# Kernel optimization log

Measured on AMD Instinct MI355X. Metric: run time of the kernel, lower is better.

The kernel has to match this reference:

```python
import jax, jax.numpy as jnp
import numpy as np

D_MODEL = 1024
STATE = 16
EXPAND = 2
D_INNER = D_MODEL * EXPAND
KCONV = 4


def setup_inputs() -> dict:
    key = jax.random.key(0)
    ks = jax.random.split(key, 8)
    s = 0.02  # small init scale for stability
    return {
        "x": jax.random.normal(ks[0], (2, 2048, D_MODEL), jnp.float32),
        "W_in": jax.random.normal(ks[1], (2 * D_INNER, D_MODEL), jnp.float32) * s,
        "conv_w": jax.random.normal(ks[2], (D_INNER, 1, KCONV), jnp.float32) * s,
        "conv_b": jnp.zeros((D_INNER,), jnp.float32),
        # A negative so exp(delta*A) <= 1 (stable recurrence, as in real Mamba init)
        "A": -jnp.abs(jax.random.normal(ks[3], (D_INNER, STATE), jnp.float32)),
        "W_x": jax.random.normal(ks[4], (2 * STATE + 1, D_INNER), jnp.float32) * s,
        "W_dt": jax.random.normal(ks[5], (D_INNER, 1), jnp.float32) * s,
        "b_dt": jnp.zeros((D_INNER,), jnp.float32),
        "W_out": jax.random.normal(ks[6], (D_MODEL, D_INNER), jnp.float32) * s,
    }


def reference(x, W_in, conv_w, conv_b, A, W_x, W_dt, b_dt, W_out):
    B, L, _ = x.shape
    N = A.shape[1]

    # in_proj, split into x-branch and gate z
    xz = jnp.einsum('bld,ed->ble', x, W_in)            # (B,L,2*d_inner)
    xi, z = jnp.split(xz, 2, axis=-1)

    # causal depthwise conv1d (torch: pad=3, kernel=4, truncate to L == left-pad 3, valid)
    xc = jnp.transpose(xi, (0, 2, 1))                  # (B,d_inner,L)
    xc = jnp.pad(xc, ((0, 0), (0, 0), (KCONV - 1, 0)))
    xc = jax.lax.conv_general_dilated(
        xc, conv_w, window_strides=(1,), padding='VALID',
        dimension_numbers=('NCH', 'OIH', 'NCH'),
        feature_group_count=conv_w.shape[0])
    xc = xc + conv_b[None, :, None]
    u = jax.nn.silu(jnp.transpose(xc, (0, 2, 1)))      # (B,L,d_inner)

    # input-dependent delta, B, C
    x_dbl = jnp.einsum('bld,ed->ble', u, W_x)          # (B,L,2N+1)
    dlt, Bm, Cm = jnp.split(x_dbl, [1, 1 + N], axis=-1)
    delta = jax.nn.softplus(dlt @ W_dt.T + b_dt)       # (B,L,d_inner)

    # selective scan over time
    def step(h, inp):
        u_t, d_t, B_t, C_t = inp                       # (B,d),(B,d),(B,N),(B,N)
        A_bar = jnp.exp(d_t[..., None] * A)            # (B,d,N)
        h = A_bar * h + (d_t * u_t)[..., None] * B_t[:, None, :]
        y = jnp.einsum('bdn,bn->bd', h, C_t)
        return h, y

    h0 = jnp.zeros((B, A.shape[0], N), u.dtype)
    xs = (jnp.swapaxes(u, 0, 1), jnp.swapaxes(delta, 0, 1),
          jnp.swapaxes(Bm, 0, 1), jnp.swapaxes(Cm, 0, 1))
    _, ys = jax.lax.scan(step, h0, xs)                 # ys: (L,B,d_inner)
    y = jnp.swapaxes(ys, 0, 1)

    y = y * jax.nn.silu(z)
    return jnp.einsum('bld,md->blm', y, W_out)
```

## Files before the change

kernel.cpp:

```cpp
#include <hip/hip_runtime.h>
#include <hip/hip_bf16.h>

#define BATCH   2
#define LSEQ    2048
#define DMODEL  1024
#define DINNER  2048
#define NST     16

#define LC      32
#define NCHUNK  (LSEQ / LC)

#define LOG2E   1.4426950408889634f
#define RLOG2E  0.6931471805599453f

typedef __bf16 bf16x8 __attribute__((ext_vector_type(8)));
typedef float  f32x4  __attribute__((ext_vector_type(4)));

__device__ __forceinline__ unsigned short f2bf(float f) {
  unsigned int u = __float_as_uint(f);
  return (unsigned short)((u + 0x7FFFu + ((u >> 16) & 1u)) >> 16);
}

__device__ __forceinline__ float fast_exp2(float x) {
#if __has_builtin(__builtin_amdgcn_exp2f)
  return __builtin_amdgcn_exp2f(x);
#else
  float r; asm("v_exp_f32 %0, %1\ns_nop 0" : "=v"(r) : "v"(x)); return r;
#endif
}
__device__ __forceinline__ float fast_log2(float x) {
#if __has_builtin(__builtin_amdgcn_logf)
  return __builtin_amdgcn_logf(x);
#else
  float r; asm("v_log_f32 %0, %1\ns_nop 0" : "=v"(r) : "v"(x)); return r;
#endif
}
__device__ __forceinline__ float fast_softplus(float x) {
  float ex = fast_exp2(x * LOG2E);
  return fast_log2(1.0f + ex) * RLOG2E;
}

__device__ __forceinline__ void async_copy16(const void* g, void* l) {
  __builtin_amdgcn_global_load_lds((__attribute__((address_space(1))) void*)g,
                                   (__attribute__((address_space(3))) void*)l,
                                   16, 0, 0);
}

__global__ __launch_bounds__(256) void cvt_tri(const float4* __restrict__ a,
                                               ushort4* __restrict__ oa, int na4,
                                               const float4* __restrict__ b,
                                               ushort4* __restrict__ ob, int nb4,
                                               const float4* __restrict__ c,
                                               ushort4* __restrict__ oc, int nc4) {
  int i = blockIdx.x * 256 + threadIdx.x;
  if (i < na4) {
    float4 v = a[i];
    ushort4 r; r.x = f2bf(v.x); r.y = f2bf(v.y); r.z = f2bf(v.z); r.w = f2bf(v.w);
    oa[i] = r;
  } else if (i - na4 < nb4) {
    int j = i - na4;
    float4 v = b[j];
    ushort4 r; r.x = f2bf(v.x); r.y = f2bf(v.y); r.z = f2bf(v.z); r.w = f2bf(v.w);
    ob[j] = r;
  } else if (i - na4 - nb4 < nc4) {
    int j = i - na4 - nb4;
    float4 v = c[j];
    ushort4 r; r.x = f2bf(v.x); r.y = f2bf(v.y); r.z = f2bf(v.z); r.w = f2bf(v.w);
    oc[j] = r;
  }
}

template<int N, int BN, int K, int NSPLIT>
__global__ __launch_bounds__(256, 2) void gemm_bf16(const unsigned short* __restrict__ A,
                                                    const unsigned short* __restrict__ B,
                                                    float* __restrict__ C0,
                                                    float* __restrict__ C1) {
  constexpr int NB = BN / 32;
  __shared__ unsigned short As[128][64];
  __shared__ unsigned short Bs[BN][64];
  const int tid  = threadIdx.x;
  const int wave = tid >> 6;
  const int lane = tid & 63;
  const int row0 = blockIdx.y * 128;
  const int col0 = blockIdx.x * BN;
  const int wr   = (wave >> 1) * 64;
  const int wc   = (wave & 1)  * (BN / 2);
  const int fr   = lane & 15;
  const int fq   = lane >> 4;

  f32x4 acc[4][NB] = {};

  const int sr  = wave * 8 + (lane >> 3);
  const int gp  = lane & 7;
  const int sgl = gp ^ (sr & 7);
  const unsigned short* gA = A + (size_t)(row0 + sr) * K + sgl * 8;
  const unsigned short* gB = B + (size_t)(col0 + sr) * K + sgl * 8;
  char* lA = (char*)As + wave * 1024;
  char* lB = (char*)Bs + wave * 1024;

  const int rsw = (fr & 7);

  for (int k0 = 0; k0 < K; k0 += 64) {
    #pragma unroll
    for (int c = 0; c < 4; ++c)
      async_copy16(gA + (size_t)c * 32 * K + k0, lA + c * 4096);
    #pragma unroll
    for (int c = 0; c < NB; ++c)
      async_copy16(gB + (size_t)c * 32 * K + k0, lB + c * 4096);
    __syncthreads();

    #pragma unroll
    for (int kk = 0; kk < 2; ++kk) {
      bf16x8 af[4], bfr[NB];
      #pragma unroll
      for (int i = 0; i < 4; ++i)
        af[i] = *(const bf16x8*)((const char*)As + (wr + i * 16 + fr) * 128 +
                                 (((kk << 2) | fq) ^ rsw) * 16);
      #pragma unroll
      for (int j = 0; j < NB; ++j)
        bfr[j] = *(const bf16x8*)((const char*)Bs + (wc + j * 16 + fr) * 128 +
                                  (((kk << 2) | fq) ^ rsw) * 16);
      #pragma unroll
      for (int i = 0; i < 4; ++i)
        #pragma unroll
        for (int j = 0; j < NB; ++j)
          acc[i][j] = __builtin_amdgcn_mfma_f32_16x16x32_bf16(af[i], bfr[j], acc[i][j], 0, 0, 0);
    }
    __syncthreads();
  }

  float* Cb;
  int cb, cstride;
  if (col0 < NSPLIT) { Cb = C0; cb = col0;          cstride = NSPLIT; }
  else               { Cb = C1; cb = col0 - NSPLIT; cstride = N - NSPLIT; }

  #pragma unroll
  for (int i = 0; i < 4; ++i)
    #pragma unroll
    for (int j = 0; j < NB; ++j) {
      int row = row0 + wr + i * 16 + fq * 4;
      int col = cb + wc + j * 16 + fr;
      #pragma unroll
      for (int r = 0; r < 4; ++r)
        Cb[(size_t)(row + r) * cstride + col] = acc[i][j][r];
    }
}

__global__ __launch_bounds__(256) void conv_kernel(const float* __restrict__ xi,
                                                   const float* __restrict__ cw,
                                                   const float* __restrict__ cb,
                                                   float* __restrict__ u) {
  size_t i = (size_t)blockIdx.x * 256 + threadIdx.x;
  int d4 = (int)(i & (DINNER / 4 - 1));
  int t2 = (int)((i >> 9) & (LSEQ / 2 - 1));
  int b  = (int)(i >> 19);
  int d  = d4 * 4;
  int t0 = t2 * 2;

  float4 w0 = *(const float4*)(cw + (d + 0) * 4);
  float4 w1 = *(const float4*)(cw + (d + 1) * 4);
  float4 w2 = *(const float4*)(cw + (d + 2) * 4);
  float4 w3 = *(const float4*)(cw + (d + 3) * 4);
  float4 bias = *(const float4*)(cb + d);

  size_t base = ((size_t)b * LSEQ + t0) * DINNER + d;
  const float4 zero = make_float4(0.f, 0.f, 0.f, 0.f);
  float4 xm3 = (t0 >= 3) ? *(const float4*)(xi + base - 3 * DINNER) : zero;
  float4 xm2 = (t0 >= 2) ? *(const float4*)(xi + base - 2 * DINNER) : zero;
  float4 xm1 = (t0 >= 1) ? *(const float4*)(xi + base - 1 * DINNER) : zero;
  float4 x00 = *(const float4*)(xi + base);
  float4 xp1 = *(const float4*)(xi + base + DINNER);

  float4 s0, s1;
  s0.x = bias.x + w0.x * xm3.x + w0.y * xm2.x + w0.z * xm1.x + w0.w * x00.x;
  s0.y = bias.y + w1.x * xm3.y + w1.y * xm2.y + w1.z * xm1.y + w1.w * x00.y;
  s0.z = bias.z + w2.x * xm3.z + w2.y * xm2.z + w2.z * xm1.z + w2.w * x00.z;
  s0.w = bias.w + w3.x * xm3.w + w3.y * xm2.w + w3.z * xm1.w + w3.w * x00.w;
  s1.x = bias.x + w0.x * xm2.x + w0.y * xm1.x + w0.z * x00.x + w0.w * xp1.x;
  s1.y = bias.y + w1.x * xm2.y + w1.y * xm1.y + w1.z * x00.y + w1.w * xp1.y;
  s1.z = bias.z + w2.x * xm2.z + w2.y * xm1.z + w2.z * x00.z + w2.w * xp1.z;
  s1.w = bias.w + w3.x * xm2.w + w3.y * xm1.w + w3.z * x00.w + w3.w * xp1.w;

  float4 r0, r1;
  r0.x = s0.x / (1.0f + __expf(-s0.x));
  r0.y = s0.y / (1.0f + __expf(-s0.y));
  r0.z = s0.z / (1.0f + __expf(-s0.z));
  r0.w = s0.w / (1.0f + __expf(-s0.w));
  r1.x = s1.x / (1.0f + __expf(-s1.x));
  r1.y = s1.y / (1.0f + __expf(-s1.y));
  r1.z = s1.z / (1.0f + __expf(-s1.z));
  r1.w = s1.w / (1.0f + __expf(-s1.w));

  *(float4*)(u + base)          = r0;
  *(float4*)(u + base + DINNER) = r1;
}

__global__ __launch_bounds__(256, 2) void xdbl_kernel(const float* __restrict__ u,
                                                      const float* __restrict__ Wx,
                                                      float* __restrict__ dltbuf,
                                                      float* __restrict__ bc) {
  const int tid  = threadIdx.x;
  const int wave = tid >> 6;
  const int lane = tid & 63;
  const int row0 = blockIdx.x * 4;

  float acc[9][4];
  #pragma unroll
  for (int i = 0; i < 9; ++i)
    #pragma unroll
    for (int r = 0; r < 4; ++r) acc[i][r] = 0.0f;

  const float* up    = u  + (size_t)row0 * DINNER + lane * 4;
  const float* wbase = Wx + (size_t)wave * 8 * DINNER + lane * 4;
  const float* w32   = Wx + (size_t)32 * DINNER + lane * 4;

  for (int kt = 0; kt < 8; ++kt) {
    const int ko = kt * 256;
    float4 uv0 = *(const float4*)(up + 0 * DINNER + ko);
    float4 uv1 = *(const float4*)(up + 1 * DINNER + ko);
    float4 uv2 = *(const float4*)(up + 2 * DINNER + ko);
    float4 uv3 = *(const float4*)(up + 3 * DINNER + ko);
    #pragma unroll
    for (int i = 0; i < 9; ++i) {
      float4 w = (i < 8) ? *(const float4*)(wbase + (size_t)i * DINNER + ko)
                         : *(const float4*)(w32 + ko);
      acc[i][0] = fmaf(uv0.x, w.x, fmaf(uv0.y, w.y, fmaf(uv0.z, w.z, fmaf(uv0.w, w.w, acc[i][0]))));
      acc[i][1] = fmaf(uv1.x, w.x, fmaf(uv1.y, w.y, fmaf(uv1.z, w.z, fmaf(uv1.w, w.w, acc[i][1]))));
      acc[i][2] = fmaf(uv2.x, w.x, fmaf(uv2.y, w.y, fmaf(uv2.z, w.z, fmaf(uv2.w, w.w, acc[i][2]))));
      acc[i][3] = fmaf(uv3.x, w.x, fmaf(uv3.y, w.y, fmaf(uv3.z, w.z, fmaf(uv3.w, w.w, acc[i][3]))));
    }
  }

  #pragma unroll
  for (int i = 0; i < 9; ++i)
    #pragma unroll
    for (int r = 0; r < 4; ++r)
      #pragma unroll
      for (int m = 1; m < 64; m <<= 1)
        acc[i][r] += __shfl_xor(acc[i][r], m);

  #pragma unroll
  for (int r = 0; r < 4; ++r) {
    if (lane == r) {
      const size_t row = row0 + r;
      #pragma unroll
      for (int i = 0; i < 8; ++i) {
        const int e = wave * 8 + i;
        if (e == 0) dltbuf[row] = acc[i][r];
        else        bc[row * 32 + (e - 1)] = acc[i][r];
      }
      if (wave == 0) bc[row * 32 + 31] = acc[8][r];
    }
  }
}

__global__ __launch_bounds__(256) void scanA(const float* __restrict__ u,
                                             const float* __restrict__ dltbuf,
                                             const float* __restrict__ bc,
                                             const float* __restrict__ Amat,
                                             const float* __restrict__ Wdt,
                                             const float* __restrict__ bdt,
                                             float* __restrict__ Sbuf,
                                             float* __restrict__ Wbuf) {
  __shared__ float sB[LC][16];
  __shared__ float sdlt[LC];
  const int tid  = threadIdx.x;
  const int dblk = blockIdx.x & 7;
  const int c    = (blockIdx.x >> 3) & (NCHUNK - 1);
  const int b    = blockIdx.x >> 9;
  const int d    = dblk * 256 + tid;
  const int t0   = c * LC;

  if (tid < LC * 4) {
    int r = tid >> 2, cp = (tid & 3) * 4;
    *(float4*)&sB[r][cp] = *(const float4*)(bc + ((size_t)(b * LSEQ + t0) + r) * 32 + cp);
  }
  if (tid < LC) sdlt[tid] = dltbuf[(size_t)b * LSEQ + t0 + tid];

  const float wd = Wdt[d];
  const float bd = bdt[d];
  float A2[16];
  #pragma unroll
  for (int i = 0; i < 4; ++i) {
    float4 v = *(const float4*)(Amat + (size_t)d * 16 + i * 4);
    A2[i*4+0] = v.x * LOG2E; A2[i*4+1] = v.y * LOG2E;
    A2[i*4+2] = v.z * LOG2E; A2[i*4+3] = v.w * LOG2E;
  }
  float h[16];
  #pragma unroll
  for (int n = 0; n < 16; ++n) h[n] = 0.0f;
  float S = 0.0f;

  size_t gu = ((size_t)b * LSEQ + t0) * DINNER + d;
  float u0 = u[gu], u1 = u[gu + DINNER];
  __syncthreads();

  auto body = [&](float uc, int ttl) {
    float dl = fast_softplus(fmaf(sdlt[ttl], wd, bd));
    float Bv[16];
    *(float4*)&Bv[0]  = *(const float4*)&sB[ttl][0];
    *(float4*)&Bv[4]  = *(const float4*)&sB[ttl][4];
    *(float4*)&Bv[8]  = *(const float4*)&sB[ttl][8];
    *(float4*)&Bv[12] = *(const float4*)&sB[ttl][12];
    S += dl;
    float dlu = dl * uc;
    #pragma unroll
    for (int n = 0; n < 16; ++n) {
      float ab = fast_exp2(dl * A2[n]);
      h[n] = fmaf(ab, h[n], dlu * Bv[n]);
    }
  };

  for (int tt = 0; tt < LC; tt += 2) {
    float u2 = u[gu + 2 * DINNER], u3 = u[gu + 3 * DINNER];
    body(u0, tt);
    body(u1, tt + 1);
    u0 = u2; u1 = u3;
    gu += 2 * DINNER;
  }

  const size_t gc = (size_t)(b * DINNER + d);
  Sbuf[gc * NCHUNK + c] = S;
  size_t o = (gc * NCHUNK + c) * 16;
  #pragma unroll
  for (int i = 0; i < 4; ++i)
    *(float4*)(Wbuf + o + i * 4) = make_float4(h[i*4], h[i*4+1], h[i*4+2], h[i*4+3]);
}

__global__ __launch_bounds__(256) void scanB(const float* __restrict__ Sbuf,
                                             float* __restrict__ Wbuf,
                                             const float* __restrict__ Amat) {
  const int lane_id = blockIdx.x * 256 + threadIdx.x;
  const int gc = lane_id >> 4;
  const int n  = lane_id & 15;
  const int d  = gc & (DINNER - 1);
  const float A2 = Amat[(size_t)d * 16 + n] * LOG2E;
  const float* sp = Sbuf + (size_t)gc * NCHUNK;
  const size_t wbase = (size_t)gc * NCHUNK * 16 + n;
  float h = 0.0f;
  #pragma unroll 8
  for (int c = 0; c < NCHUNK; ++c) {
    float P = fast_exp2(A2 * sp[c]);
    float hin = h;
    h = fmaf(P, h, Wbuf[wbase + (size_t)c * 16]);
    Wbuf[wbase + (size_t)c * 16] = hin;
  }
}

__global__ __launch_bounds__(256) void scanC(const float* __restrict__ u,
                                             const float* __restrict__ zz,
                                             const float* __restrict__ dltbuf,
                                             const float* __restrict__ bc,
                                             const float* __restrict__ Amat,
                                             const float* __restrict__ Wdt,
                                             const float* __restrict__ bdt,
                                             const float* __restrict__ Hin,
                                             unsigned short* __restrict__ ybf) {
  __shared__ float sbc[LC][32];
  __shared__ float sdlt[LC];
  const int tid  = threadIdx.x;
  const int dblk = blockIdx.x & 7;
  const int c    = (blockIdx.x >> 3) & (NCHUNK - 1);
  const int b    = blockIdx.x >> 9;
  const int d    = dblk * 256 + tid;
  const int t0   = c * LC;

  ((float4*)sbc)[tid] = ((const float4*)(bc + ((size_t)b * LSEQ + t0) * 32))[tid];
  if (tid < LC) sdlt[tid] = dltbuf[(size_t)b * LSEQ + t0 + tid];

  const float wd = Wdt[d];
  const float bd = bdt[d];
  float A2[16];
  #pragma unroll
  for (int i = 0; i < 4; ++i) {
    float4 v = *(const float4*)(Amat + (size_t)d * 16 + i * 4);
    A2[i*4+0] = v.x * LOG2E; A2[i*4+1] = v.y * LOG2E;
    A2[i*4+2] = v.z * LOG2E; A2[i*4+3] = v.w * LOG2E;
  }
  const size_t o = ((size_t)(b * DINNER + d) * NCHUNK + c) * 16;
  float h[16];
  #pragma unroll
  for (int i = 0; i < 4; ++i) {
    float4 v = *(const float4*)(Hin + o + i * 4);
    h[i*4+0] = v.x; h[i*4+1] = v.y; h[i*4+2] = v.z; h[i*4+3] = v.w;
  }

  size_t gu = ((size_t)b * LSEQ + t0) * DINNER + d;

  float u0 = u[gu],  u1 = u[gu + DINNER];
  float z0 = zz[gu], z1 = zz[gu + DINNER];
  __syncthreads();

  auto body = [&](float uc, float zc, int ttl, size_t cu) {
    float dl = fast_softplus(fmaf(sdlt[ttl], wd, bd));
    float Bv[16], Cv[16];
    *(float4*)&Bv[0]  = *(const float4*)&sbc[ttl][0];
    *(float4*)&Bv[4]  = *(const float4*)&sbc[ttl][4];
    *(float4*)&Bv[8]  = *(const float4*)&sbc[ttl][8];
    *(float4*)&Bv[12] = *(const float4*)&sbc[ttl][12];
    *(float4*)&Cv[0]  = *(const float4*)&sbc[ttl][16];
    *(float4*)&Cv[4]  = *(const float4*)&sbc[ttl][20];
    *(float4*)&Cv[8]  = *(const float4*)&sbc[ttl][24];
    *(float4*)&Cv[12] = *(const float4*)&sbc[ttl][28];
    float dlu = dl * uc;
    float y = 0.0f;
    #pragma unroll
    for (int n = 0; n < 16; ++n) {
      float ab = fast_exp2(dl * A2[n]);
      h[n] = fmaf(ab, h[n], dlu * Bv[n]);
      y = fmaf(h[n], Cv[n], y);
    }
    float sig = 1.0f / (1.0f + __expf(-zc));
    ybf[cu] = f2bf(y * zc * sig);
  };

  for (int tt = 0; tt < LC; tt += 2) {
    float u2 = u[gu + 2 * DINNER],  u3 = u[gu + 3 * DINNER];
    float z2 = zz[gu + 2 * DINNER], z3 = zz[gu + 3 * DINNER];
    body(u0, z0, tt,     gu);
    body(u1, z1, tt + 1, gu + DINNER);
    u0 = u2; u1 = u3; z0 = z2; z1 = z3;
    gu += 2 * DINNER;
  }
}

extern "C" void kernel_launch(void* const* d_in, const int* in_sizes, int n_in,
                              void* d_out, int out_size, void* d_ws, size_t ws_size,
                              hipStream_t stream) {
  const float* x      = (const float*)d_in[0];
  const float* W_in   = (const float*)d_in[1];
  const float* conv_w = (const float*)d_in[2];
  const float* conv_b = (const float*)d_in[3];
  const float* A      = (const float*)d_in[4];
  const float* W_x    = (const float*)d_in[5];
  const float* W_dt   = (const float*)d_in[6];
  const float* b_dt   = (const float*)d_in[7];
  const float* W_out  = (const float*)d_in[8];
  float* out = (float*)d_out;

  float* ws  = (float*)d_ws;
  float* xi  = ws;
  float* zz  = xi  + (size_t)BATCH * LSEQ * DINNER;
  float* u   = zz  + (size_t)BATCH * LSEQ * DINNER;
  float* bc  = u   + (size_t)BATCH * LSEQ * DINNER;
  float* Sb  = bc  + (size_t)BATCH * LSEQ * 32;
  float* dlt = Sb  + (size_t)BATCH * DINNER * NCHUNK;
  float* Wb  = dlt + (size_t)BATCH * LSEQ;

  const int ML = BATCH * LSEQ;

  unsigned short* x_bf    = (unsigned short*)Wb;
  unsigned short* win_bf  = (unsigned short*)Wb + (size_t)ML * DMODEL;
  unsigned short* ybf     = (unsigned short*)xi;
  unsigned short* wout_bf = (unsigned short*)(Wb + (size_t)BATCH * DINNER * NCHUNK * 16);

  const int na4 = ML * DMODEL / 4, nb4 = 2 * DINNER * DMODEL / 4, nc4 = DMODEL * DINNER / 4;
  cvt_tri<<<(na4 + nb4 + nc4 + 255) / 256, 256, 0, stream>>>(
      (const float4*)x, (ushort4*)x_bf, na4,
      (const float4*)W_in, (ushort4*)win_bf, nb4,
      (const float4*)W_out, (ushort4*)wout_bf, nc4);
  gemm_bf16<2 * DINNER, 128, DMODEL, DINNER><<<dim3((2 * DINNER) / 128, ML / 128), 256, 0, stream>>>(
      x_bf, win_bf, xi, zz);
  conv_kernel<<<(ML * DINNER / 8) / 256, 256, 0, stream>>>(xi, conv_w, conv_b, u);
  xdbl_kernel<<<ML / 4, 256, 0, stream>>>(u, W_x, dlt, bc);
  scanA<<<BATCH * NCHUNK * 8, 256, 0, stream>>>(u, dlt, bc, A, W_dt, b_dt, Sb, Wb);
  scanB<<<(BATCH * DINNER * NST) / 256, 256, 0, stream>>>(Sb, Wb, A);
  scanC<<<BATCH * NCHUNK * 8, 256, 0, stream>>>(u, zz, dlt, bc, A, W_dt, b_dt, Wb, ybf);
  gemm_bf16<DMODEL, 32, DINNER, DMODEL><<<dim3(DMODEL / 32, ML / 128), 256, 0, stream>>>(
      ybf, wout_bf, out, out);
}
```

Baseline: 198.1 us.

## Replace in_proj GEMM with 256x256-tile 8-wave double-buffered async-LDS kernel

Adds a new bf16 MFMA GEMM for the input projection. It uses 512 threads, 256x256 output tiles, an XOR-swizzled LDS layout, and two 32-deep K stages filled by global_load_lds async copies, with explicit waitcnt, barriers and setprio around the MFMA bursts. The larger tile raises data reuse per LDS load and the double buffering overlaps global loads with compute, cutting memory traffic and stalls in the largest GEMM. In exchange the grid shrinks to 256 blocks at one block per CU, and the 64KB LDS plus 128 accumulator registers per thread limit occupancy.

```diff
diff --git a/kernel.cpp b/kernel.cpp
--- a/kernel.cpp
+++ b/kernel.cpp
@@ -45,6 +45,8 @@
                                    (__attribute__((address_space(3))) void*)l,
                                    16, 0, 0);
 }
+
+#define SCHED0 __builtin_amdgcn_sched_barrier(0)
 
 __global__ __launch_bounds__(256) void cvt_tri(const float4* __restrict__ a,
                                                ushort4* __restrict__ oa, int na4,
@@ -70,6 +72,115 @@
   }
 }
 
+__global__ __launch_bounds__(512, 1) void gemm8p(const unsigned short* __restrict__ A,
+                                                 const unsigned short* __restrict__ B,
+                                                 float* __restrict__ C0,
+                                                 float* __restrict__ C1) {
+  constexpr int K = 1024;
+  __shared__ char lds[65536];
+  const int tid  = threadIdx.x;
+  const int lane = tid & 63;
+  const int wave = tid >> 6;
+  const int fr   = lane & 15;
+  const int fq   = lane >> 4;
+  const int wr   = (wave >> 2) * 128;
+  const int wc   = (wave & 3) * 64;
+  const int row0 = blockIdx.y * 256;
+  const int col0 = blockIdx.x * 256;
+
+  f32x4 acc[8][4] = {};
+
+  const int i0 = tid, i1 = tid + 512;
+  const int r0 = i0 >> 2, g0 = i0 & 3;
+  const int r1 = i1 >> 2, g1 = i1 & 3;
+  const unsigned short* gA0 = A + (size_t)(row0 + r0) * K + (g0 ^ (r0 & 3)) * 8;
+  const unsigned short* gA1 = A + (size_t)(row0 + r1) * K + (g1 ^ (r1 & 3)) * 8;
+  const unsigned short* gB0 = B + (size_t)(col0 + r0) * K + (g0 ^ (r0 & 3)) * 8;
+  const unsigned short* gB1 = B + (size_t)(col0 + r1) * K + (g1 ^ (r1 & 3)) * 8;
+  char* const dA0 = lds + (i0 - lane) * 16;
+  char* const dA1 = lds + (i1 - lane) * 16;
+  char* const dB0 = lds + 16384 + (i0 - lane) * 16;
+  char* const dB1 = lds + 16384 + (i1 - lane) * 16;
+
+  auto STAGE = [&](int kt, int sb) {
+    const int k0 = kt * 32;
+    async_copy16(gA0 + k0, dA0 + sb);
+    async_copy16(gA1 + k0, dA1 + sb);
+    async_copy16(gB0 + k0, dB0 + sb);
+    async_copy16(gB1 + k0, dB1 + sb);
+  };
+
+  const int swz = (fq ^ (fr & 3)) * 16;
+  auto COMPUTE = [&](int sb) {
+    const char* LA = lds + sb;
+    const char* LB = lds + sb + 16384;
+    bf16x8 bfrg[4], afrg[4];
+    #pragma unroll
+    for (int j = 0; j < 4; ++j)
+      bfrg[j] = *(const bf16x8*)(LB + (wc + j * 16 + fr) * 64 + swz);
+    #pragma unroll
+    for (int i = 0; i < 4; ++i)
+      afrg[i] = *(const bf16x8*)(LA + (wr + i * 16 + fr) * 64 + swz);
+    __builtin_amdgcn_s_setprio(1);
+    #pragma unroll
+    for (int i = 0; i < 4; ++i)
+      #pragma unroll
+      for (int j = 0; j < 4; ++j)
+        acc[i][j] = __builtin_amdgcn_mfma_f32_16x16x32_bf16(afrg[i], bfrg[j], acc[i][j], 0, 0, 0);
+    __builtin_amdgcn_s_setprio(0);
+    #pragma unroll
+    for (int i = 0; i < 4; ++i)
+      afrg[i] = *(const bf16x8*)(LA + (wr + (i + 4) * 16 + fr) * 64 + swz);
+    __builtin_amdgcn_s_setprio(1);
+    #pragma unroll
+    for (int i = 0; i < 4; ++i)
+      #pragma unroll
+      for (int j = 0; j < 4; ++j)
+        acc[i + 4][j] = __builtin_amdgcn_mfma_f32_16x16x32_bf16(afrg[i], bfrg[j], acc[i + 4][j], 0, 0, 0);
+    __builtin_amdgcn_s_setprio(0);
+  };
+
+  STAGE(0, 0);
+  STAGE(1, 32768);
+  asm volatile("s_waitcnt vmcnt(4)" ::: "memory"); SCHED0;
+  __builtin_amdgcn_s_barrier(); SCHED0;
+
+  for (int tp = 0; tp < 16; ++tp) {
+    COMPUTE(0);
+    __builtin_amdgcn_s_barrier(); SCHED0;
+    if (tp < 15) {
+      STAGE(2 * tp + 2, 0);
+      asm volatile("s_waitcnt vmcnt(4)" ::: "memory");
+    } else {
+      asm volatile("s_waitcnt vmcnt(0)" ::: "memory");
+    }
+    SCHED0;
+    __builtin_amdgcn_s_barrier(); SCHED0;
+
+    COMPUTE(32768);
+    if (tp == 15) break;
+    __builtin_amdgcn_s_barrier(); SCHED0;
+    STAGE(2 * tp + 3, 32768);
+    asm volatile("s_waitcnt vmcnt(4)" ::: "memory");
+    SCHED0;
+    __builtin_amdgcn_s_barrier(); SCHED0;
+  }
+
+  float* Cb; int cb;
+  if (col0 < DINNER) { Cb = C0; cb = col0; }
+  else               { Cb = C1; cb = col0 - DINNER; }
+  #pragma unroll
+  for (int i = 0; i < 8; ++i)
+    #pragma unroll
+    for (int j = 0; j < 4; ++j) {
+      int row = row0 + wr + i * 16 + fq * 4;
+      int col = cb + wc + j * 16 + fr;
+      #pragma unroll
+      for (int r = 0; r < 4; ++r)
+        Cb[(size_t)(row + r) * DINNER + col] = acc[i][j][r];
+    }
+}
+
 template<int N, int BN, int K, int NSPLIT>
 __global__ __launch_bounds__(256, 2) void gemm_bf16(const unsigned short* __restrict__ A,
                                                     const unsigned short* __restrict__ B,
@@ -459,8 +570,7 @@
       (const float4*)x, (ushort4*)x_bf, na4,
       (const float4*)W_in, (ushort4*)win_bf, nb4,
       (const float4*)W_out, (ushort4*)wout_bf, nc4);
-  gemm_bf16<2 * DINNER, 128, DMODEL, DINNER><<<dim3((2 * DINNER) / 128, ML / 128), 256, 0, stream>>>(
-      x_bf, win_bf, xi, zz);
+  gemm8p<<<dim3(16, 16), 512, 0, stream>>>(x_bf, win_bf, xi, zz);
   conv_kernel<<<(ML * DINNER / 8) / 256, 256, 0, stream>>>(xi, conv_w, conv_b, u);
   xdbl_kernel<<<ML / 4, 256, 0, stream>>>(u, W_x, dlt, bc);
   scanA<<<BATCH * NCHUNK * 8, 256, 0, stream>>>(u, dlt, bc, A, W_dt, b_dt, Sb, Wb);
```

After: 202.4 us. 2.2% more time.

## Fuse causal depthwise conv and SiLU into in_proj GEMM epilogue

Applied to the files above, without the earlier changes.

The in_proj GEMM epilogue now applies the causal depthwise conv and SiLU directly on the accumulator tile, using lane shuffles to fetch the three previous timesteps within each 64-row tile. Only the boundary rows at tile edges are stored raw, and a small conv_fix kernel recomputes the first three rows of each 64-row tile. This removes the full fp32 xi write and reread plus the separate conv pass. In exchange the epilogue does more ALU work and makes scattered partial stores, and correctness depends on the cross-wave boundary bookkeeping.

```diff
diff --git a/kernel.cpp b/kernel.cpp
--- a/kernel.cpp
+++ b/kernel.cpp
@@ -38,6 +38,10 @@
 __device__ __forceinline__ float fast_softplus(float x) {
   float ex = fast_exp2(x * LOG2E);
   return fast_log2(1.0f + ex) * RLOG2E;
+}
+
+__device__ __forceinline__ float silu(float x) {
+  return x / (1.0f + __expf(-x));
 }
 
 __device__ __forceinline__ void async_copy16(const void* g, void* l) {
@@ -70,11 +74,14 @@
   }
 }
 
-template<int N, int BN, int K, int NSPLIT>
+template<int N, int BN, int K, int NSPLIT, bool FUSE>
 __global__ __launch_bounds__(256, 2) void gemm_bf16(const unsigned short* __restrict__ A,
                                                     const unsigned short* __restrict__ B,
                                                     float* __restrict__ C0,
-                                                    float* __restrict__ C1) {
+                                                    float* __restrict__ C1,
+                                                    const float* __restrict__ cw,
+                                                    const float* __restrict__ cbs,
+                                                    float* __restrict__ xiraw) {
   constexpr int NB = BN / 32;
   __shared__ unsigned short As[128][64];
   __shared__ unsigned short Bs[BN][64];
@@ -129,70 +136,99 @@
     __syncthreads();
   }
 
-  float* Cb;
-  int cb, cstride;
-  if (col0 < NSPLIT) { Cb = C0; cb = col0;          cstride = NSPLIT; }
-  else               { Cb = C1; cb = col0 - NSPLIT; cstride = N - NSPLIT; }
-
-  #pragma unroll
-  for (int i = 0; i < 4; ++i)
+  if (FUSE && col0 < NSPLIT) {
+    const int src = (lane + 48) & 63;
     #pragma unroll
     for (int j = 0; j < NB; ++j) {
-      int row = row0 + wr + i * 16 + fq * 4;
-      int col = cb + wc + j * 16 + fr;
-      #pragma unroll
-      for (int r = 0; r < 4; ++r)
-        Cb[(size_t)(row + r) * cstride + col] = acc[i][j][r];
+      const int d = col0 + wc + j * 16 + fr;
+      const float4 w = *(const float4*)(cw + d * 4);
+      const float cb0 = cbs[d];
+      float pr1 = 0.f, pr2 = 0.f, pr3 = 0.f;
+      #pragma unroll
+      for (int i = 0; i < 4; ++i) {
+        float a0 = acc[i][j][0], a1 = acc[i][j][1];
+        float a2 = acc[i][j][2], a3 = acc[i][j][3];
+        float e1 = (fq == 3) ? pr1 : a1;
+        float e2 = (fq == 3) ? pr2 : a2;
+        float e3 = (fq == 3) ? pr3 : a3;
+        float xm1 = __shfl(e3, src);
+        float xm2 = __shfl(e2, src);
+        float xm3 = __shfl(e1, src);
+        const int rowq = row0 + wr + i * 16 + fq * 4;
+        float c0v = cb0 + w.x * xm3 + w.y * xm2 + w.z * xm1 + w.w * a0;
+        float c1v = cb0 + w.x * xm2 + w.y * xm1 + w.z * a0  + w.w * a1;
+        float c2v = cb0 + w.x * xm1 + w.y * a0  + w.z * a1  + w.w * a2;
+        float c3v = cb0 + w.x * a0  + w.y * a1  + w.z * a2  + w.w * a3;
+        C0[(size_t)(rowq + 0) * NSPLIT + d] = silu(c0v);
+        C0[(size_t)(rowq + 1) * NSPLIT + d] = silu(c1v);
+        C0[(size_t)(rowq + 2) * NSPLIT + d] = silu(c2v);
+        C0[(size_t)(rowq + 3) * NSPLIT + d] = silu(c3v);
+        if (i == 0 && fq == 0) {
+          xiraw[(size_t)(rowq + 0) * NSPLIT + d] = a0;
+          xiraw[(size_t)(rowq + 1) * NSPLIT + d] = a1;
+          xiraw[(size_t)(rowq + 2) * NSPLIT + d] = a2;
+        }
+        if (i == 3 && fq == 3) {
+          xiraw[(size_t)(rowq + 1) * NSPLIT + d] = a1;
+          xiraw[(size_t)(rowq + 2) * NSPLIT + d] = a2;
+          xiraw[(size_t)(rowq + 3) * NSPLIT + d] = a3;
+        }
+        pr1 = a1; pr2 = a2; pr3 = a3;
+      }
     }
-}
-
-__global__ __launch_bounds__(256) void conv_kernel(const float* __restrict__ xi,
-                                                   const float* __restrict__ cw,
-                                                   const float* __restrict__ cb,
-                                                   float* __restrict__ u) {
-  size_t i = (size_t)blockIdx.x * 256 + threadIdx.x;
-  int d4 = (int)(i & (DINNER / 4 - 1));
-  int t2 = (int)((i >> 9) & (LSEQ / 2 - 1));
-  int b  = (int)(i >> 19);
-  int d  = d4 * 4;
-  int t0 = t2 * 2;
+  } else {
+    float* Cb;
+    int cb, cstride;
+    if (col0 < NSPLIT) { Cb = C0; cb = col0;          cstride = NSPLIT; }
+    else               { Cb = C1; cb = col0 - NSPLIT; cstride = N - NSPLIT; }
+    #pragma unroll
+    for (int i = 0; i < 4; ++i)
+      #pragma unroll
+      for (int j = 0; j < NB; ++j) {
+        int row = row0 + wr + i * 16 + fq * 4;
+        int col = cb + wc + j * 16 + fr;
+        #pragma unroll
+        for (int r = 0; r < 4; ++r)
+          Cb[(size_t)(row + r) * cstride + col] = acc[i][j][r];
+      }
+  }
+}
+
+__global__ __launch_bounds__(256) void conv_fix(const float* __restrict__ xiraw,
+                                                const float* __restrict__ cw,
+                                                const float* __restrict__ cbs,
+                                                float* __restrict__ u) {
+  int idx = blockIdx.x * 256 + threadIdx.x;
+  int d4  = idx & 511;
+  int rr  = idx >> 9;
+  int k   = rr / 3;
+  int rho = rr - k * 3;
+  int q   = k * 64 + rho;
+  int t   = q & (LSEQ - 1);
+  int d   = d4 * 4;
 
   float4 w0 = *(const float4*)(cw + (d + 0) * 4);
   float4 w1 = *(const float4*)(cw + (d + 1) * 4);
   float4 w2 = *(const float4*)(cw + (d + 2) * 4);
   float4 w3 = *(const float4*)(cw + (d + 3) * 4);
-  float4 bias = *(const float4*)(cb + d);
-
-  size_t base = ((size_t)b * LSEQ + t0) * DINNER + d;
+  float4 bias = *(const float4*)(cbs + d);
+
+  size_t base = (size_t)q * DINNER + d;
   const float4 zero = make_float4(0.f, 0.f, 0.f, 0.f);
-  float4 xm3 = (t0 >= 3) ? *(const float4*)(xi + base - 3 * DINNER) : zero;
-  float4 xm2 = (t0 >= 2) ? *(const float4*)(xi + base - 2 * DINNER) : zero;
-  float4 xm1 = (t0 >= 1) ? *(const float4*)(xi + base - 1 * DINNER) : zero;
-  float4 x00 = *(const float4*)(xi + base);
-  float4 xp1 = *(const float4*)(xi + base + DINNER);
-
-  float4 s0, s1;
-  s0.x = bias.x + w0.x * xm3.x + w0.y * xm2.x + w0.z * xm1.x + w0.w * x00.x;
-  s0.y = bias.y + w1.x * xm3.y + w1.y * xm2.y + w1.z * xm1.y + w1.w * x00.y;
-  s0.z = bias.z + w2.x * xm3.z + w2.y * xm2.z + w2.z * xm1.z + w2.w * x00.z;
-  s0.w = bias.w + w3.x * xm3.w + w3.y * xm2.w + w3.z * xm1.w + w3.w * x00.w;
-  s1.x = bias.x + w0.x * xm2.x + w0.y * xm1.x + w0.z * x00.x + w0.w * xp1.x;
-  s1.y = bias.y + w1.x * xm2.y + w1.y * xm1.y + w1.z * x00.y + w1.w * xp1.y;
-  s1.z = bias.z + w2.x * xm2.z + w2.y * xm1.z + w2.z * x00.z + w2.w * xp1.z;
-  s1.w = bias.w + w3.x * xm2.w + w3.y * xm1.w + w3.z * x00.w + w3.w * xp1.w;
-
-  float4 r0, r1;
-  r0.x = s0.x / (1.0f + __expf(-s0.x));
-  r0.y = s0.y / (1.0f + __expf(-s0.y));
-  r0.z = s0.z / (1.0f + __expf(-s0.z));
-  r0.w = s0.w / (1.0f + __expf(-s0.w));
-  r1.x = s1.x / (1.0f + __expf(-s1.x));
-  r1.y = s1.y / (1.0f + __expf(-s1.y));
-  r1.z = s1.z / (1.0f + __expf(-s1.z));
-  r1.w = s1.w / (1.0f + __expf(-s1.w));
-
-  *(float4*)(u + base)          = r0;
-  *(float4*)(u + base + DINNER) = r1;
+  float4 xm3 = (t >= 3) ? *(const float4*)(xiraw + base - 3 * DINNER) : zero;
+  float4 xm2 = (t >= 2) ? *(const float4*)(xiraw + base - 2 * DINNER) : zero;
+  float4 xm1 = (t >= 1) ? *(const float4*)(xiraw + base - 1 * DINNER) : zero;
+  float4 x00 = *(const float4*)(xiraw + base);
+
+  float4 s;
+  s.x = bias.x + w0.x * xm3.x + w0.y * xm2.x + w0.z * xm1.x + w0.w * x00.x;
+  s.y = bias.y + w1.x * xm3.y + w1.y * xm2.y + w1.z * xm1.y + w1.w * x00.y;
+  s.z = bias.z + w2.x * xm3.z + w2.y * xm2.z + w2.z * xm1.z + w2.w * x00.z;
+  s.w = bias.w + w3.x * xm3.w + w3.y * xm2.w + w3.z * xm1.w + w3.w * x00.w;
+
+  float4 r;
+  r.x = silu(s.x); r.y = silu(s.y); r.z = silu(s.z); r.w = silu(s.w);
+  *(float4*)(u + base) = r;
 }
 
 __global__ __launch_bounds__(256, 2) void xdbl_kernel(const float* __restrict__ u,
@@ -459,13 +495,15 @@
       (const float4*)x, (ushort4*)x_bf, na4,
       (const float4*)W_in, (ushort4*)win_bf, nb4,
       (const float4*)W_out, (ushort4*)wout_bf, nc4);
-  gemm_bf16<2 * DINNER, 128, DMODEL, DINNER><<<dim3((2 * DINNER) / 128, ML / 128), 256, 0, stream>>>(
-      x_bf, win_bf, xi, zz);
-  conv_kernel<<<(ML * DINNER / 8) / 256, 256, 0, stream>>>(xi, conv_w, conv_b, u);
+  gemm_bf16<2 * DINNER, 128, DMODEL, DINNER, true>
+      <<<dim3((2 * DINNER) / 128, ML / 128), 256, 0, stream>>>(
+      x_bf, win_bf, u, zz, conv_w, conv_b, xi);
+  conv_fix<<<(64 * 3 * 512) / 256, 256, 0, stream>>>(xi, conv_w, conv_b, u);
   xdbl_kernel<<<ML / 4, 256, 0, stream>>>(u, W_x, dlt, bc);
   scanA<<<BATCH * NCHUNK * 8, 256, 0, stream>>>(u, dlt, bc, A, W_dt, b_dt, Sb, Wb);
   scanB<<<(BATCH * DINNER * NST) / 256, 256, 0, stream>>>(Sb, Wb, A);
   scanC<<<BATCH * NCHUNK * 8, 256, 0, stream>>>(u, zz, dlt, bc, A, W_dt, b_dt, Wb, ybf);
-  gemm_bf16<DMODEL, 32, DINNER, DMODEL><<<dim3(DMODEL / 32, ML / 128), 256, 0, stream>>>(
-      ybf, wout_bf, out, out);
-}
+  gemm_bf16<DMODEL, 32, DINNER, DMODEL, false>
+      <<<dim3(DMODEL / 32, ML / 128), 256, 0, stream>>>(
+      ybf, wout_bf, out, out, conv_w, conv_b, u);
+}
```

New measurement: 183.1 us. -7.6%, faster.
